# Kernel tuning notes

Measured on AMD Instinct MI355X. Metric: run time of the kernel, lower is better.

Reference implementation:

```python
import jax, jax.numpy as jnp
import numpy as np

B, C, H, W = 256, 1024, 7, 7
D_HID, N_CLS = 768, 5

def setup_inputs() -> dict:
    key = jax.random.key(0)
    k1, k2, k3, k4, k5 = jax.random.split(key, 5)
    flat = C * H * W  # 50176
    return {
        "features": jax.random.normal(k1, (B, C, H, W), dtype=jnp.float32),
        "W1": jax.random.normal(k2, (D_HID, flat), dtype=jnp.float32) * 0.02,
        "b1": jax.random.normal(k3, (D_HID,), dtype=jnp.float32) * 0.02,
        "W2": jax.random.normal(k4, (N_CLS, D_HID), dtype=jnp.float32) * 0.02,
        "b2": jax.random.normal(k5, (N_CLS,), dtype=jnp.float32) * 0.02,
    }

def reference(features, W1, b1, W2, b2):
    # PCAM: per-(batch, channel) global max over spatial dims, broadcast-multiplied
    # back onto the feature map. Replaces the torch Python double loop with one
    # fused reduce-max + elementwise multiply.
    ch_max = jnp.max(features, axis=(2, 3), keepdims=True)  # [B, C, 1, 1]
    pcams = features * ch_max                               # [B, C, H, W]
    flat = pcams.reshape(pcams.shape[0], -1)                # [B, C*H*W]
    h = jax.nn.relu(flat @ W1.T + b1)                       # [B, 768]
    logits = h @ W2.T + b2                                  # [B, num_classes]
    return (logits, features)
```

## Files before the change

### kernel.cpp

```cpp
#include <hip/hip_runtime.h>
#include <hip/hip_bf16.h>

#define B_SZ   256
#define C_SZ   1024
#define HW     49
#define KDIM   50176
#define DHID   768
#define NCLS   5

typedef __bf16 bf16x8 __attribute__((ext_vector_type(8)));
typedef __bf16 bf16x4 __attribute__((ext_vector_type(4)));
typedef float  f32x4  __attribute__((ext_vector_type(4)));

__global__ __launch_bounds__(256) void pcam_kernel(const float* __restrict__ feat,
                                                   float* __restrict__ feat_out,
                                                   __bf16* __restrict__ pcam) {
  __shared__ float sv[1568];
  __shared__ float smax[32];
  const int tid = threadIdx.x;
  const size_t base = (size_t)blockIdx.x * 1568;

  const float4* src4 = (const float4*)(feat + base);
  float4* dst4 = (float4*)(feat_out + base);
  #pragma unroll
  for (int i = 0; i < 2; ++i) {
    int idx = tid + i * 256;
    if (idx < 392) {
      float4 v = src4[idx];
      dst4[idx] = v;
      ((float4*)sv)[idx] = v;
    }
  }
  __syncthreads();

  {
    const int r = tid >> 3, p = tid & 7;
    float mx = -INFINITY;
    for (int i = p; i < HW; i += 8) mx = fmaxf(mx, sv[r * HW + i]);
    #pragma unroll
    for (int off = 1; off < 8; off <<= 1) mx = fmaxf(mx, __shfl_xor(mx, off));
    if (p == 0) smax[r] = mx;
  }
  __syncthreads();

  for (int i = tid; i < 1568; i += 256) {
    int r = (i * 1338) >> 16;
    float v = sv[i] * smax[r];
    pcam[base + i] = (__bf16)v;
  }
}

#define BM 128
#define BN 128
#define BK 64
#define MT 2
#define NT 6
#define KSPLIT 42
#define KSTEPS 784

__global__ __launch_bounds__(512, 4) void gemm1_kernel(const __bf16* __restrict__ pcam,
                                                       const float* __restrict__ W1,
                                                       float* __restrict__ h_part) {
  __shared__ __bf16 Asm[2][BM * BK];
  __shared__ __bf16 Bsm[2][BN * BK];

  const int tid  = threadIdx.x;
  const int lane = tid & 63;
  const int w    = tid >> 6;
  const int wm   = w >> 2;
  const int wn   = w & 3;
  const int bx   = blockIdx.x;
  const int m0   = (bx & 1) * BM;
  const int n0   = (bx >> 1) * BN;
  const int ks   = blockIdx.y;
  const int s0   = (ks * KSTEPS) / KSPLIT;
  const int s1   = ((ks + 1) * KSTEPS) / KSPLIT;

  const int nb  = tid >> 4;
  const int kq  = tid & 15;
  const int kb  = kq >> 1;
  const int sub = (kq & 1) << 3;
  const int ma  = tid >> 2;
  const int kb0 = (tid & 3) * 2;

  const float* wbase = W1 + (size_t)(n0 + nb) * KDIM + kq * 4;
  const __bf16* abase = pcam + (size_t)(m0 + ma) * KDIM + kb0 * 8;

  f32x4 acc[4][2];
  #pragma unroll
  for (int i = 0; i < 4; ++i)
    #pragma unroll
    for (int j = 0; j < 2; ++j) acc[i][j] = f32x4{0.f, 0.f, 0.f, 0.f};

  float4 bA0, bA1, bA2, bA3;
  float4 bB0, bB1, bB2, bB3;
  bf16x8 ar0, ar1;

#define LOAD_B(R0, R1, R2, R3, s) do { \
    const size_t ko_ = (size_t)(s) * BK; \
    R0 = *(const float4*)(wbase + ko_); \
    R1 = *(const float4*)(wbase + (size_t)32 * KDIM + ko_); \
    R2 = *(const float4*)(wbase + (size_t)64 * KDIM + ko_); \
    R3 = *(const float4*)(wbase + (size_t)96 * KDIM + ko_); \
  } while (0)

#define LOAD_A(s) do { \
    const __bf16* p_ = abase + (size_t)(s) * BK; \
    ar0 = *(const bf16x8*)(p_); \
    ar1 = *(const bf16x8*)(p_ + 8); \
  } while (0)

#define WRITE_B(bi, R0, R1, R2, R3) do { \
    _Pragma("unroll") \
    for (int it = 0; it < 4; ++it) { \
      const float4 v = (it == 0) ? R0 : (it == 1) ? R1 : (it == 2) ? R2 : R3; \
      bf16x4 bv; \
      bv[0] = (__bf16)v.x; bv[1] = (__bf16)v.y; bv[2] = (__bf16)v.z; bv[3] = (__bf16)v.w; \
      const int n = it * 32 + nb; \
      const int phys = n * 128 + (((kb ^ (n & 7)) << 4) | sub); \
      *(bf16x4*)((char*)Bsm[bi] + phys) = bv; \
    } \
  } while (0)

#define WRITE_A(bi) do { \
    const int p0 = ma * 128 + (((kb0 ^ (ma & 7)) << 4)); \
    const int p1 = ma * 128 + ((((kb0 + 1) ^ (ma & 7)) << 4)); \
    *(bf16x8*)((char*)Asm[bi] + p0) = ar0; \
    *(bf16x8*)((char*)Asm[bi] + p1) = ar1; \
  } while (0)

#define COMPUTE(bi) do { \
    _Pragma("unroll") \
    for (int ksub = 0; ksub < 2; ++ksub) { \
      bf16x8 af[4], bfr[2]; \
      const int kb2 = ksub * 4 + (lane >> 4); \
      _Pragma("unroll") \
      for (int i = 0; i < 4; ++i) { \
        const int m = wm * 64 + i * 16 + (lane & 15); \
        af[i] = *(const bf16x8*)((const char*)Asm[bi] + m * 128 + ((kb2 ^ (m & 7)) << 4)); \
      } \
      _Pragma("unroll") \
      for (int j = 0; j < 2; ++j) { \
        const int n = wn * 32 + j * 16 + (lane & 15); \
        bfr[j] = *(const bf16x8*)((const char*)Bsm[bi] + n * 128 + ((kb2 ^ (n & 7)) << 4)); \
      } \
      _Pragma("unroll") \
      for (int i = 0; i < 4; ++i) \
        _Pragma("unroll") \
        for (int j = 0; j < 2; ++j) \
          acc[i][j] = __builtin_amdgcn_mfma_f32_16x16x32_bf16(af[i], bfr[j], acc[i][j], 0, 0, 0); \
    } \
  } while (0)

  LOAD_B(bA0, bA1, bA2, bA3, s0);
  if (s0 + 1 < s1) LOAD_B(bB0, bB1, bB2, bB3, s0 + 1);
  LOAD_A(s0);
  WRITE_B(s0 & 1, bA0, bA1, bA2, bA3);
  WRITE_A(s0 & 1);
  if (s0 + 1 < s1) LOAD_A(s0 + 1);
  __syncthreads();

  for (int s = s0; s < s1; ++s) {
    const int cur = s & 1;
    const int rel = (s ^ s0) & 1;
    if (s + 2 < s1) {
      if (rel) LOAD_B(bB0, bB1, bB2, bB3, s + 2);
      else     LOAD_B(bA0, bA1, bA2, bA3, s + 2);
    }
    if (s + 1 < s1) {
      if (rel) WRITE_B(cur ^ 1, bA0, bA1, bA2, bA3);
      else     WRITE_B(cur ^ 1, bB0, bB1, bB2, bB3);
    }
    COMPUTE(cur);
    if (s + 1 < s1) WRITE_A(cur ^ 1);
    if (s + 2 < s1) LOAD_A(s + 2);
    __syncthreads();
  }

  float* out = h_part + (size_t)ks * DHID * B_SZ;
  #pragma unroll
  for (int i = 0; i < 4; ++i) {
    const int mb = m0 + wm * 64 + i * 16 + (lane >> 4) * 4;
    #pragma unroll
    for (int j = 0; j < 2; ++j) {
      const int n = n0 + wn * 32 + j * 16 + (lane & 15);
      *(f32x4*)(out + (size_t)n * B_SZ + mb) = acc[i][j];
    }
  }
#undef LOAD_B
#undef LOAD_A
#undef WRITE_B
#undef WRITE_A
#undef COMPUTE
}

__global__ __launch_bounds__(256) void reduce_kernel(const float* __restrict__ h_part,
                                                     const float* __restrict__ b1,
                                                     float* __restrict__ h) {
  const int n = blockIdx.x;
  const int m = threadIdx.x;
  float s = 0.f;
  #pragma unroll 6
  for (int ks = 0; ks < KSPLIT; ++ks)
    s += h_part[((size_t)ks * DHID + n) * B_SZ + m];
  float v = s + b1[n];
  h[(size_t)m * DHID + n] = v > 0.f ? v : 0.f;
}

__global__ __launch_bounds__(64) void head_kernel(const float* __restrict__ h,
                                                  const float* __restrict__ W2,
                                                  const float* __restrict__ b2,
                                                  float* __restrict__ logits) {
  const int m = blockIdx.x;
  const int lane = threadIdx.x;
  float hv[12];
  #pragma unroll
  for (int j = 0; j < 12; ++j) hv[j] = h[(size_t)m * DHID + j * 64 + lane];
  #pragma unroll
  for (int c = 0; c < NCLS; ++c) {
    float s = 0.f;
    #pragma unroll
    for (int j = 0; j < 12; ++j) s += hv[j] * W2[c * DHID + j * 64 + lane];
    #pragma unroll
    for (int off = 32; off > 0; off >>= 1) s += __shfl_xor(s, off);
    if (lane == 0) logits[m * NCLS + c] = s + b2[c];
  }
}

extern "C" void kernel_launch(void* const* d_in, const int* in_sizes, int n_in,
                              void* d_out, int out_size, void* d_ws, size_t ws_size,
                              hipStream_t stream) {
  const float* feat = (const float*)d_in[0];
  const float* W1   = (const float*)d_in[1];
  const float* b1   = (const float*)d_in[2];
  const float* W2   = (const float*)d_in[3];
  const float* b2   = (const float*)d_in[4];

  float* logits   = (float*)d_out;
  float* feat_out = (float*)d_out + (size_t)B_SZ * NCLS;

  char* ws = (char*)d_ws;
  __bf16* pcam   = (__bf16*)ws;
  float*  h_part = (float*)(ws + (size_t)B_SZ * KDIM * 2);
  float*  h      = (float*)(ws + (size_t)B_SZ * KDIM * 2
                               + (size_t)KSPLIT * DHID * B_SZ * 4);

  pcam_kernel<<<(B_SZ * C_SZ) / 32, 256, 0, stream>>>(feat, feat_out, pcam);
  gemm1_kernel<<<dim3(MT * NT, KSPLIT), 512, 0, stream>>>(pcam, W1, h_part);
  reduce_kernel<<<DHID, 256, 0, stream>>>(h_part, b1, h);
  head_kernel<<<B_SZ, 64, 0, stream>>>(h, W2, b2, logits);
}
```

Measured before the change: 107.9 us.

## Use direct global-to-LDS loads with triple-buffered pipeline in GEMM1

Replaces the register-staged global loads and manual LDS writes in the split-K GEMM with global_load_lds DMA-style loads into a three-buffer ring, halving BK to 32. W1 is now kept as fp32 in LDS and converted to bf16 at fragment-read time instead of before the LDS store. The aim is to cut VGPR pressure and VALU store work and keep two tiles in flight. In exchange it doubles the number of barriers per unit of K, doubles LDS bytes for B, and does the conversion redundantly across waves.

```diff
diff --git a/kernel.cpp b/kernel.cpp
--- a/kernel.cpp
+++ b/kernel.cpp
@@ -9,8 +9,11 @@
 #define NCLS   5
 
 typedef __bf16 bf16x8 __attribute__((ext_vector_type(8)));
-typedef __bf16 bf16x4 __attribute__((ext_vector_type(4)));
 typedef float  f32x4  __attribute__((ext_vector_type(4)));
+
+#define GLOAD_LDS16(gsrc, ldst) \
+  __builtin_amdgcn_global_load_lds((__attribute__((address_space(1))) void*)(gsrc), \
+                                   (__attribute__((address_space(3))) void*)(ldst), 16, 0, 0)
 
 __global__ __launch_bounds__(256) void pcam_kernel(const float* __restrict__ feat,
                                                    float* __restrict__ feat_out,
@@ -52,17 +55,18 @@
 
 #define BM 128
 #define BN 128
-#define BK 64
+#define BK 32
+#define NBUF 3
 #define MT 2
 #define NT 6
 #define KSPLIT 42
-#define KSTEPS 784
+#define KSTEPS 1568
 
 __global__ __launch_bounds__(512, 4) void gemm1_kernel(const __bf16* __restrict__ pcam,
                                                        const float* __restrict__ W1,
                                                        float* __restrict__ h_part) {
-  __shared__ __bf16 Asm[2][BM * BK];
-  __shared__ __bf16 Bsm[2][BN * BK];
+  __shared__ __bf16 Asm[NBUF][BM * BK];
+  __shared__ float  Bsm[NBUF][BN * BK];
 
   const int tid  = threadIdx.x;
   const int lane = tid & 63;
@@ -76,15 +80,17 @@
   const int s0   = (ks * KSTEPS) / KSPLIT;
   const int s1   = ((ks + 1) * KSTEPS) / KSPLIT;
 
-  const int nb  = tid >> 4;
-  const int kq  = tid & 15;
-  const int kb  = kq >> 1;
-  const int sub = (kq & 1) << 3;
-  const int ma  = tid >> 2;
-  const int kb0 = (tid & 3) * 2;
-
-  const float* wbase = W1 + (size_t)(n0 + nb) * KDIM + kq * 4;
-  const __bf16* abase = pcam + (size_t)(m0 + ma) * KDIM + kb0 * 8;
+  const int m_d = w * 16 + (lane >> 2);
+  const int ua  = (lane & 3) ^ (m_d & 3);
+  const __bf16* asrc = pcam + (size_t)(m0 + m_d) * KDIM + ua * 8;
+
+  const int r1  = w * 8 + (lane >> 3);
+  const int ub  = (lane & 7) ^ (r1 & 7);
+  const float* bsrc1 = W1 + (size_t)(n0 + r1) * KDIM + ub * 4;
+  const float* bsrc2 = W1 + (size_t)(n0 + 64 + r1) * KDIM + ub * 4;
+
+  char* aw = (char*)&Asm[0][0] + w * 1024;
+  char* bw = (char*)&Bsm[0][0] + w * 1024;
 
   f32x4 acc[4][2];
   #pragma unroll
@@ -92,89 +98,58 @@
     #pragma unroll
     for (int j = 0; j < 2; ++j) acc[i][j] = f32x4{0.f, 0.f, 0.f, 0.f};
 
-  float4 bA0, bA1, bA2, bA3;
-  float4 bB0, bB1, bB2, bB3;
-  bf16x8 ar0, ar1;
-
-#define LOAD_B(R0, R1, R2, R3, s) do { \
+#define ISSUE(bi, s) do { \
     const size_t ko_ = (size_t)(s) * BK; \
-    R0 = *(const float4*)(wbase + ko_); \
-    R1 = *(const float4*)(wbase + (size_t)32 * KDIM + ko_); \
-    R2 = *(const float4*)(wbase + (size_t)64 * KDIM + ko_); \
-    R3 = *(const float4*)(wbase + (size_t)96 * KDIM + ko_); \
+    GLOAD_LDS16(asrc + ko_,  aw + (size_t)(bi) * (BM * BK * 2)); \
+    GLOAD_LDS16(bsrc1 + ko_, bw + (size_t)(bi) * (BN * BK * 4)); \
+    GLOAD_LDS16(bsrc2 + ko_, bw + (size_t)(bi) * (BN * BK * 4) + 8192); \
   } while (0)
 
-#define LOAD_A(s) do { \
-    const __bf16* p_ = abase + (size_t)(s) * BK; \
-    ar0 = *(const bf16x8*)(p_); \
-    ar1 = *(const bf16x8*)(p_ + 8); \
+#define COMPUTE(bi) do { \
+    const int j_  = lane >> 4; \
+    const int c_  = lane & 15; \
+    bf16x8 af[4]; \
+    _Pragma("unroll") \
+    for (int i = 0; i < 4; ++i) { \
+      const int m = wm * 64 + i * 16 + c_; \
+      af[i] = *(const bf16x8*)((const char*)Asm[bi] + m * 64 + ((j_ ^ (m & 3)) << 4)); \
+    } \
+    bf16x8 bfr[2]; \
+    _Pragma("unroll") \
+    for (int jf = 0; jf < 2; ++jf) { \
+      const int n = wn * 32 + jf * 16 + c_; \
+      const f32x4 b0 = *(const f32x4*)((const char*)Bsm[bi] + n * 128 + (((2 * j_)     ^ (n & 7)) << 4)); \
+      const f32x4 b1 = *(const f32x4*)((const char*)Bsm[bi] + n * 128 + (((2 * j_ + 1) ^ (n & 7)) << 4)); \
+      bfr[jf][0] = (__bf16)b0[0]; bfr[jf][1] = (__bf16)b0[1]; \
+      bfr[jf][2] = (__bf16)b0[2]; bfr[jf][3] = (__bf16)b0[3]; \
+      bfr[jf][4] = (__bf16)b1[0]; bfr[jf][5] = (__bf16)b1[1]; \
+      bfr[jf][6] = (__bf16)b1[2]; bfr[jf][7] = (__bf16)b1[3]; \
+    } \
+    _Pragma("unroll") \
+    for (int i = 0; i < 4; ++i) \
+      _Pragma("unroll") \
+      for (int jf = 0; jf < 2; ++jf) \
+        acc[i][jf] = __builtin_amdgcn_mfma_f32_16x16x32_bf16(af[i], bfr[jf], acc[i][jf], 0, 0, 0); \
   } while (0)
 
-#define WRITE_B(bi, R0, R1, R2, R3) do { \
-    _Pragma("unroll") \
-    for (int it = 0; it < 4; ++it) { \
-      const float4 v = (it == 0) ? R0 : (it == 1) ? R1 : (it == 2) ? R2 : R3; \
-      bf16x4 bv; \
-      bv[0] = (__bf16)v.x; bv[1] = (__bf16)v.y; bv[2] = (__bf16)v.z; bv[3] = (__bf16)v.w; \
-      const int n = it * 32 + nb; \
-      const int phys = n * 128 + (((kb ^ (n & 7)) << 4) | sub); \
-      *(bf16x4*)((char*)Bsm[bi] + phys) = bv; \
-    } \
-  } while (0)
-
-#define WRITE_A(bi) do { \
-    const int p0 = ma * 128 + (((kb0 ^ (ma & 7)) << 4)); \
-    const int p1 = ma * 128 + ((((kb0 + 1) ^ (ma & 7)) << 4)); \
-    *(bf16x8*)((char*)Asm[bi] + p0) = ar0; \
-    *(bf16x8*)((char*)Asm[bi] + p1) = ar1; \
-  } while (0)
-
-#define COMPUTE(bi) do { \
-    _Pragma("unroll") \
-    for (int ksub = 0; ksub < 2; ++ksub) { \
-      bf16x8 af[4], bfr[2]; \
-      const int kb2 = ksub * 4 + (lane >> 4); \
-      _Pragma("unroll") \
-      for (int i = 0; i < 4; ++i) { \
-        const int m = wm * 64 + i * 16 + (lane & 15); \
-        af[i] = *(const bf16x8*)((const char*)Asm[bi] + m * 128 + ((kb2 ^ (m & 7)) << 4)); \
-      } \
-      _Pragma("unroll") \
-      for (int j = 0; j < 2; ++j) { \
-        const int n = wn * 32 + j * 16 + (lane & 15); \
-        bfr[j] = *(const bf16x8*)((const char*)Bsm[bi] + n * 128 + ((kb2 ^ (n & 7)) << 4)); \
-      } \
-      _Pragma("unroll") \
-      for (int i = 0; i < 4; ++i) \
-        _Pragma("unroll") \
-        for (int j = 0; j < 2; ++j) \
-          acc[i][j] = __builtin_amdgcn_mfma_f32_16x16x32_bf16(af[i], bfr[j], acc[i][j], 0, 0, 0); \
-    } \
-  } while (0)
-
-  LOAD_B(bA0, bA1, bA2, bA3, s0);
-  if (s0 + 1 < s1) LOAD_B(bB0, bB1, bB2, bB3, s0 + 1);
-  LOAD_A(s0);
-  WRITE_B(s0 & 1, bA0, bA1, bA2, bA3);
-  WRITE_A(s0 & 1);
-  if (s0 + 1 < s1) LOAD_A(s0 + 1);
-  __syncthreads();
+  int b0i = 0, b1i = 1, b2i = 2;
+  ISSUE(0, s0);
+  if (s0 + 1 < s1) ISSUE(1, s0 + 1);
 
   for (int s = s0; s < s1; ++s) {
-    const int cur = s & 1;
-    const int rel = (s ^ s0) & 1;
     if (s + 2 < s1) {
-      if (rel) LOAD_B(bB0, bB1, bB2, bB3, s + 2);
-      else     LOAD_B(bA0, bA1, bA2, bA3, s + 2);
+      ISSUE(b2i, s + 2);
+      asm volatile("s_waitcnt vmcnt(6)" ::: "memory");
+    } else if (s + 1 < s1) {
+      asm volatile("s_waitcnt vmcnt(3)" ::: "memory");
+    } else {
+      asm volatile("s_waitcnt vmcnt(0)" ::: "memory");
     }
-    if (s + 1 < s1) {
-      if (rel) WRITE_B(cur ^ 1, bA0, bA1, bA2, bA3);
-      else     WRITE_B(cur ^ 1, bB0, bB1, bB2, bB3);
-    }
-    COMPUTE(cur);
-    if (s + 1 < s1) WRITE_A(cur ^ 1);
-    if (s + 2 < s1) LOAD_A(s + 2);
-    __syncthreads();
+    __builtin_amdgcn_s_barrier();
+    COMPUTE(b0i);
+    asm volatile("s_waitcnt lgkmcnt(0)" ::: "memory");
+    __builtin_amdgcn_s_barrier();
+    const int t = b0i; b0i = b1i; b1i = b2i; b2i = t;
   }
 
   float* out = h_part + (size_t)ks * DHID * B_SZ;
@@ -187,10 +162,7 @@
       *(f32x4*)(out + (size_t)n * B_SZ + mb) = acc[i][j];
     }
   }
-#undef LOAD_B
-#undef LOAD_A
-#undef WRITE_B
-#undef WRITE_A
+#undef ISSUE
 #undef COMPUTE
 }
 
```

Result: slower. 110.4 us (+2.3%).
